# Kernel optimization log

Hardware: AMD Instinct MI355X
Metric: run time of the kernel (lower is better)

Reference implementation:

```python
import jax, jax.numpy as jnp
import numpy as np

V, E, H, B, S, T = 32000, 256, 256, 64, 512, 256


def setup_inputs() -> dict:
    key = jax.random.key(0)
    ks = jax.random.split(key, 24)
    def w(i, shape, scale=0.05):
        return jax.random.normal(ks[i], shape, jnp.float32) * scale
    return {
        "pre_seq": jax.random.randint(ks[0], (B, S), 0, V),
        "post_seq": jax.random.randint(ks[1], (B, S), 0, V),
        "trg": jax.random.randint(ks[2], (B, T), 0, V),
        "emb": w(3, (V, E)),
        "Wi_pre": w(4, (3 * H, E)), "Wh_pre": w(5, (3 * H, H)),
        "bi_pre": w(6, (3 * H,)), "bh_pre": w(7, (3 * H,)),
        "Wi_post": w(8, (3 * H, E)), "Wh_post": w(9, (3 * H, H)),
        "bi_post": w(10, (3 * H,)), "bh_post": w(11, (3 * H,)),
        "Wfc": w(12, (H, 2 * H)), "bfc": w(13, (H,)),
        "Wi_dec": w(14, (3 * H, E)), "Wh_dec": w(15, (3 * H, H)),
        "bi_dec": w(16, (3 * H,)), "bh_dec": w(17, (3 * H,)),
        "w_hid": w(18, (1, 2 * H)), "b_hid": w(19, (1,)),
        "w_out": w(20, (1, 1)), "b_out": w(21, (1,)),
    }


def gru_cell(h, x, Wi, Wh, bi, bh):
    # torch nn.GRU gating convention, gates ordered (r, z, n)
    gi = x @ Wi.T + bi              # (B, 3H)
    gh = h @ Wh.T + bh              # (B, 3H)
    ir, iz, inn = jnp.split(gi, 3, axis=-1)
    hr, hz, hn = jnp.split(gh, 3, axis=-1)
    r = jax.nn.sigmoid(ir + hr)
    z = jax.nn.sigmoid(iz + hz)
    n = jnp.tanh(inn + r * hn)
    return (1.0 - z) * n + z * h


def gru_seq(seq_emb, Wi, Wh, bi, bh):
    # seq_emb: (B, L, E) -> outputs (B, L, H), final hidden (B, H)
    h0 = jnp.zeros((seq_emb.shape[0], Wh.shape[1]), seq_emb.dtype)
    def step(h, x):
        h = gru_cell(h, x, Wi, Wh, bi, bh)
        return h, h
    hT, outs = jax.lax.scan(step, h0, jnp.swapaxes(seq_emb, 0, 1))
    return jnp.swapaxes(outs, 0, 1), hT


def reference(pre_seq, post_seq, trg, emb, Wi_pre, Wh_pre, bi_pre, bh_pre,
              Wi_post, Wh_post, bi_post, bh_post, Wfc, bfc,
              Wi_dec, Wh_dec, bi_dec, bh_dec, w_hid, b_hid, w_out, b_out):
    # Encoder: two GRUs over pre/post token embeddings (dropout off / eval mode)
    pre_out, pre_h = gru_seq(emb[pre_seq], Wi_pre, Wh_pre, bi_pre, bh_pre)
    post_out, post_h = gru_seq(emb[post_seq], Wi_post, Wh_post, bi_post, bh_post)
    enc_out = jnp.concatenate([pre_out, post_out], axis=1)          # (B, 2S, H)
    h0 = jnp.tanh(jnp.concatenate([pre_h, post_h], axis=-1) @ Wfc.T + bfc)  # (B, H)

    # fc_hid(relu(cat([enc_out, h_t]))) splits into a step-constant enc term
    # and a per-step hidden term since relu acts elementwise on the concat.
    A = jax.nn.relu(enc_out) @ w_hid[0, :H]                         # (B, 2S)

    # Teacher-forced decoder inputs: last pre token, then trg[:, :-1]
    in_toks = jnp.concatenate([pre_seq[:, -1:], trg[:, :-1]], axis=1)  # (B, T)

    def step(h, tok):
        x = emb[tok]                                                # (B, E)
        h = gru_cell(h, x, Wi_dec, Wh_dec, bi_dec, bh_dec)          # (B, H)
        s = jax.nn.relu(h) @ w_hid[0, H:]                           # (B,)
        out = (A + s[:, None] + b_hid[0]) * w_out[0, 0] + b_out[0]  # (B, 2S)
        return h, out

    _, outs = jax.lax.scan(step, h0, in_toks.T)                     # (T, B, 2S)
    outs = jnp.swapaxes(outs, 0, 1)                                 # (B, T, 2S)
    return outs[:, :, :S], outs[:, :, S:]
```

## Files before the change

kernel.cpp:

```cpp
#include <hip/hip_runtime.h>
#include <stdint.h>

typedef _Float16 f16;
typedef _Float16 half2_t __attribute__((ext_vector_type(2)));
typedef _Float16 half8_t __attribute__((ext_vector_type(8)));
typedef float    f32x4_t __attribute__((ext_vector_type(4)));
typedef uint32_t u32x32  __attribute__((ext_vector_type(32)));

constexpr int NB = 64, NS = 512, NT = 256, NE = 256, NH = 256;
constexpr int G3 = 768;

static __device__ __forceinline__ float sigm(float x){ return 1.f/(1.f+__expf(-x)); }
static __device__ __forceinline__ float tanhfast(float x){
  float e = __expf(-2.f*x);
  return (1.f-e)/(1.f+e);
}
static __device__ __forceinline__ uint32_t pack2(float a, float b){
  half2_t h; h[0]=(f16)a; h[1]=(f16)b;
  return __builtin_bit_cast(uint32_t, h);
}
static __device__ __forceinline__ float dot2f(uint32_t w, uint32_t h, float acc){
#if __has_builtin(__builtin_amdgcn_fdot2)
  return __builtin_amdgcn_fdot2(__builtin_bit_cast(half2_t,w),
                                __builtin_bit_cast(half2_t,h), acc, false);
#else
  half2_t a = __builtin_bit_cast(half2_t,w), b = __builtin_bit_cast(half2_t,h);
  return acc + (float)a[0]*(float)b[0] + (float)a[1]*(float)b[1];
#endif
}
static __device__ __forceinline__ half8_t cvt8(float4 a, float4 b){
  half8_t p;
  p[0]=(f16)a.x; p[1]=(f16)a.y; p[2]=(f16)a.z; p[3]=(f16)a.w;
  p[4]=(f16)b.x; p[5]=(f16)b.y; p[6]=(f16)b.z; p[7]=(f16)b.w;
  return p;
}

#define LOAD_W(WSRC)                                                         \
  _Pragma("unroll")                                                          \
  for (int i=0;i<32;++i){                                                    \
    wr0[i]=(WSRC)[(size_t)i*G3];          wr1[i]=(WSRC)[(size_t)(i+32)*G3];  \
    wz0[i]=(WSRC)[(size_t)i*G3+256];      wz1[i]=(WSRC)[(size_t)(i+32)*G3+256];\
    wn0[i]=(WSRC)[(size_t)i*G3+512];      wn1[i]=(WSRC)[(size_t)(i+32)*G3+512];\
  }

#define DOT_BLOCK(W_R, W_Z, W_N, HPTR)                                       \
  _Pragma("unroll")                                                          \
  for (int c=0;c<4;++c){                                                     \
    uint4 ha = *(const uint4*)((HPTR) + c*8);                                \
    uint4 hb = *(const uint4*)((HPTR) + c*8 + 4);                            \
    uint32_t hh0=ha.x,hh1=ha.y,hh2=ha.z,hh3=ha.w;                            \
    uint32_t hh4=hb.x,hh5=hb.y,hh6=hb.z,hh7=hb.w;                            \
    a0=dot2f(W_R[c*8+0],hh0,a0); a1=dot2f(W_Z[c*8+0],hh0,a1); a2=dot2f(W_N[c*8+0],hh0,a2); \
    a0=dot2f(W_R[c*8+1],hh1,a0); a1=dot2f(W_Z[c*8+1],hh1,a1); a2=dot2f(W_N[c*8+1],hh1,a2); \
    a0=dot2f(W_R[c*8+2],hh2,a0); a1=dot2f(W_Z[c*8+2],hh2,a1); a2=dot2f(W_N[c*8+2],hh2,a2); \
    a0=dot2f(W_R[c*8+3],hh3,a0); a1=dot2f(W_Z[c*8+3],hh3,a1); a2=dot2f(W_N[c*8+3],hh3,a2); \
    a0=dot2f(W_R[c*8+4],hh4,a0); a1=dot2f(W_Z[c*8+4],hh4,a1); a2=dot2f(W_N[c*8+4],hh4,a2); \
    a0=dot2f(W_R[c*8+5],hh5,a0); a1=dot2f(W_Z[c*8+5],hh5,a1); a2=dot2f(W_N[c*8+5],hh5,a2); \
    a0=dot2f(W_R[c*8+6],hh6,a0); a1=dot2f(W_Z[c*8+6],hh6,a1); a2=dot2f(W_N[c*8+6],hh6,a2); \
    a0=dot2f(W_R[c*8+7],hh7,a0); a1=dot2f(W_Z[c*8+7],hh7,a1); a2=dot2f(W_N[c*8+7],hh7,a2); \
  }

__global__ __launch_bounds__(256) void k_prep(const float* __restrict__ Wh_pre,
                                              const float* __restrict__ Wh_post,
                                              const float* __restrict__ Wh_dec,
                                              uint32_t* __restrict__ WhT_pre,
                                              uint32_t* __restrict__ WhT_post,
                                              uint32_t* __restrict__ WhT_dec,
                                              const int* __restrict__ pre_seq,
                                              const int* __restrict__ trg,
                                              int* __restrict__ in_toks){
  int bid = blockIdx.x;
  if (bid < 1152){
    const float* Wh = (bid < 384) ? Wh_pre : (bid < 768) ? Wh_post : Wh_dec;
    uint32_t* out   = (bid < 384) ? WhT_pre : (bid < 768) ? WhT_post : WhT_dec;
    int idx = (bid % 384)*256 + threadIdx.x;
    int kp = idx / G3, row = idx % G3;
    out[idx] = pack2(Wh[(size_t)row*NE + 2*kp], Wh[(size_t)row*NE + 2*kp + 1]);
  } else {
    int idx = (bid - 1152)*256 + threadIdx.x;
    int b = idx >> 8, t = idx & 255;
    in_toks[idx] = (t == 0) ? pre_seq[b*NS + NS-1] : trg[b*NT + t - 1];
  }
}

__global__ __launch_bounds__(256) void k_gemm_gi(const float* __restrict__ emb,
                                                 const int* __restrict__ toks,
                                                 const float* __restrict__ Wi,
                                                 const float* __restrict__ bi,
                                                 f16* __restrict__ out){
  __shared__ f16 As[128][72];
  __shared__ f16 Bs[128][72];
  const int tid = threadIdx.x;
  const int m0 = blockIdx.x*128, n0 = blockIdx.y*128;
  const int lane = tid & 63, wid = tid >> 6;
  const int wm = wid >> 1, wn = wid & 1;
  const int fr = lane & 15, fq = lane >> 4;

  f32x4_t acc[4][4];
  #pragma unroll
  for (int i=0;i<4;++i)
    #pragma unroll
    for (int j=0;j<4;++j){ acc[i][j][0]=0.f; acc[i][j][1]=0.f; acc[i][j][2]=0.f; acc[i][j][3]=0.f; }

  const int r = tid >> 1, hh = tid & 1;
  const int tok = toks[m0 + r];
  const float* asrc = emb + (size_t)tok*NE + hh*32;
  const float* bsrc = Wi  + (size_t)(n0 + r)*NE + hh*32;

  for (int k0 = 0; k0 < NE; k0 += 64){
    #pragma unroll
    for (int c=0;c<4;++c){
      float4 x0 = *(const float4*)(asrc + k0 + c*8);
      float4 x1 = *(const float4*)(asrc + k0 + c*8 + 4);
      *(half8_t*)&As[r][hh*32 + c*8] = cvt8(x0, x1);
      float4 y0 = *(const float4*)(bsrc + k0 + c*8);
      float4 y1 = *(const float4*)(bsrc + k0 + c*8 + 4);
      *(half8_t*)&Bs[r][hh*32 + c*8] = cvt8(y0, y1);
    }
    __syncthreads();
    #pragma unroll
    for (int kk=0; kk<2; ++kk){
      half8_t af[4], bf[4];
      #pragma unroll
      for (int m=0;m<4;++m) af[m] = *(const half8_t*)&As[wm*64 + m*16 + fr][kk*32 + fq*8];
      #pragma unroll
      for (int n=0;n<4;++n) bf[n] = *(const half8_t*)&Bs[wn*64 + n*16 + fr][kk*32 + fq*8];
      #pragma unroll
      for (int m=0;m<4;++m)
        #pragma unroll
        for (int n=0;n<4;++n)
          acc[m][n] = __builtin_amdgcn_mfma_f32_16x16x32_f16(af[m], bf[n], acc[m][n], 0,0,0);
    }
    __syncthreads();
  }
  #pragma unroll
  for (int n=0;n<4;++n){
    const int col = n0 + wn*64 + n*16 + fr;
    const float bv = bi[col];
    #pragma unroll
    for (int m=0;m<4;++m){
      const int rowb = m0 + wm*64 + m*16 + fq*4;
      #pragma unroll
      for (int j=0;j<4;++j)
        out[(size_t)(rowb + j)*G3 + col] = (f16)(acc[m][n][j] + bv);
    }
  }
}

__global__ __launch_bounds__(512, 2) void k_enc(const uint32_t* __restrict__ WhT_pre,
                                                const uint32_t* __restrict__ WhT_post,
                                                const f16* __restrict__ gi_pre,
                                                const f16* __restrict__ gi_post,
                                                const float* __restrict__ bh_pre,
                                                const float* __restrict__ bh_post,
                                                const float* __restrict__ w_hid,
                                                float* __restrict__ Abuf,
                                                float* __restrict__ preh,
                                                float* __restrict__ posth){
  __shared__ __align__(16) uint32_t h_pair[128];
  __shared__ float part[3][256];
  __shared__ float ared[4];

  const int b = blockIdx.x & 63, which = blockIdx.x >> 6;
  const int tid = threadIdx.x;
  const int n = tid & 255, half = tid >> 8;

  const uint32_t* WhT = which ? WhT_post : WhT_pre;
  const f16* gi = (which ? gi_post : gi_pre) + (size_t)b*NS*G3;
  const float* bh = which ? bh_post : bh_pre;

  u32x32 wr0, wr1, wz0, wz1, wn0, wn1;
  {
    const uint32_t* wsrc = WhT + (size_t)(half*64)*G3 + n;
    LOAD_W(wsrc);
  }
  const float bh0 = bh[n], bh1 = bh[256+n], bh2 = bh[512+n];
  const float whv = w_hid[n];
  float hreg = 0.f;
  if (tid < 128) h_pair[tid] = 0u;
  __syncthreads();

  float* Arow = Abuf + b*1024 + which*512;

  for (int t=0; t<NS; ++t){
    float g0=0.f, g1=0.f, g2=0.f;
    if (half == 0){
      const f16* gp = gi + (size_t)t*G3;
      g0 = (float)gp[n]; g1 = (float)gp[256+n]; g2 = (float)gp[512+n];
    }
    float a0=0.f, a1=0.f, a2=0.f;
    const uint32_t* hp = h_pair + half*64;
    DOT_BLOCK(wr0, wz0, wn0, hp);
    DOT_BLOCK(wr1, wz1, wn1, hp + 32);
    if (half == 1){ part[0][n]=a0; part[1][n]=a1; part[2][n]=a2; }
    __syncthreads();
    if (half == 0){
      float ghr = a0 + part[0][n] + bh0;
      float ghz = a1 + part[1][n] + bh1;
      float ghn = a2 + part[2][n] + bh2;
      float rg = sigm(g0 + ghr);
      float zg = sigm(g1 + ghz);
      float nn = tanhfast(g2 + rg*ghn);
      float hnew = (1.f - zg)*nn + zg*hreg;
      hreg = hnew;
      float hnb = __shfl_down(hnew, 1);
      if ((n & 1) == 0) h_pair[n >> 1] = pack2(hnew, hnb);
      float redv = fmaxf(hnew, 0.f) * whv;
      #pragma unroll
      for (int off=32; off; off>>=1) redv += __shfl_down(redv, off);
      if ((tid & 63) == 0) ared[tid >> 6] = redv;
    }
    __syncthreads();
    if (tid == 0) Arow[t] = ared[0]+ared[1]+ared[2]+ared[3];
  }
  if (half == 0) (which ? posth : preh)[b*NH + n] = hreg;
}

__global__ __launch_bounds__(512, 2) void k_dec(const uint32_t* __restrict__ WhT,
                                                const f16* __restrict__ gi,
                                                const float* __restrict__ bh,
                                                const float* __restrict__ w_hid,
                                                const float* __restrict__ Wfc,
                                                const float* __restrict__ bfc,
                                                const float* __restrict__ preh,
                                                const float* __restrict__ posth,
                                                float* __restrict__ sbuf){
  __shared__ __align__(16) uint32_t h_pair[128];
  __shared__ float part[3][256];
  __shared__ float ared[4];
  __shared__ float hcat[512];

  const int b = blockIdx.x;
  const int tid = threadIdx.x;
  const int n = tid & 255, half = tid >> 8;

  const float bh0 = bh[n], bh1 = bh[256+n], bh2 = bh[512+n];
  const float whv = w_hid[NH + n];
  float hreg = 0.f;

  hcat[tid] = (tid < 256) ? preh[b*NH + tid] : posth[b*NH + tid - 256];
  __syncthreads();
  {
    const float* wrow = Wfc + (size_t)n*512 + half*256;
    const float* hc = hcat + half*256;
    float acc = 0.f;
    #pragma unroll 4
    for (int j=0;j<256;j+=4){
      float4 wv = *(const float4*)(wrow + j);
      acc = fmaf(wv.x, hc[j],   acc);
      acc = fmaf(wv.y, hc[j+1], acc);
      acc = fmaf(wv.z, hc[j+2], acc);
      acc = fmaf(wv.w, hc[j+3], acc);
    }
    if (half == 1) part[0][n] = acc;
    __syncthreads();
    if (half == 0){
      float h0 = tanhfast(acc + part[0][n] + bfc[n]);
      hreg = h0;
      float hnb = __shfl_down(h0, 1);
      if ((n & 1) == 0) h_pair[n >> 1] = pack2(h0, hnb);
    }
    __syncthreads();
  }

  u32x32 wr0, wr1, wz0, wz1, wn0, wn1;
  {
    const uint32_t* wsrc = WhT + (size_t)(half*64)*G3 + n;
    LOAD_W(wsrc);
  }

  const f16* gib = gi + (size_t)b*NT*G3;
  for (int t=0; t<NT; ++t){
    float g0=0.f, g1=0.f, g2=0.f;
    if (half == 0){
      const f16* gp = gib + (size_t)t*G3;
      g0 = (float)gp[n]; g1 = (float)gp[256+n]; g2 = (float)gp[512+n];
    }
    float a0=0.f, a1=0.f, a2=0.f;
    const uint32_t* hp = h_pair + half*64;
    DOT_BLOCK(wr0, wz0, wn0, hp);
    DOT_BLOCK(wr1, wz1, wn1, hp + 32);
    if (half == 1){ part[0][n]=a0; part[1][n]=a1; part[2][n]=a2; }
    __syncthreads();
    if (half == 0){
      float ghr = a0 + part[0][n] + bh0;
      float ghz = a1 + part[1][n] + bh1;
      float ghn = a2 + part[2][n] + bh2;
      float rg = sigm(g0 + ghr);
      float zg = sigm(g1 + ghz);
      float nn = tanhfast(g2 + rg*ghn);
      float hnew = (1.f - zg)*nn + zg*hreg;
      hreg = hnew;
      float hnb = __shfl_down(hnew, 1);
      if ((n & 1) == 0) h_pair[n >> 1] = pack2(hnew, hnb);
      float redv = fmaxf(hnew, 0.f) * whv;
      #pragma unroll
      for (int off=32; off; off>>=1) redv += __shfl_down(redv, off);
      if ((tid & 63) == 0) ared[tid >> 6] = redv;
    }
    __syncthreads();
    if (tid == 0) sbuf[b*NT + t] = ared[0]+ared[1]+ared[2]+ared[3];
  }
}

__global__ __launch_bounds__(256) void k_final(const float* __restrict__ Abuf,
                                               const float* __restrict__ sbuf,
                                               const float* __restrict__ b_hid,
                                               const float* __restrict__ w_out,
                                               const float* __restrict__ b_out,
                                               float* __restrict__ out){
  const float bh = b_hid[0], wo = w_out[0], bo = b_out[0];
  const int idx = blockIdx.x*256 + threadIdx.x;
  const int j4 = idx & 127, t = (idx >> 7) & 255, b = idx >> 15;
  const float sv = sbuf[b*NT + t] + bh;
  const float4 a0 = *(const float4*)(Abuf + b*1024 + j4*4);
  const float4 a1 = *(const float4*)(Abuf + b*1024 + 512 + j4*4);
  float4 o0, o1;
  o0.x = (a0.x + sv)*wo + bo; o0.y = (a0.y + sv)*wo + bo;
  o0.z = (a0.z + sv)*wo + bo; o0.w = (a0.w + sv)*wo + bo;
  o1.x = (a1.x + sv)*wo + bo; o1.y = (a1.y + sv)*wo + bo;
  o1.z = (a1.z + sv)*wo + bo; o1.w = (a1.w + sv)*wo + bo;
  float4* o = (float4*)out;
  o[idx] = o0;
  o[(size_t)(NB*NT*NS/4) + idx] = o1;
}

extern "C" void kernel_launch(void* const* d_in, const int* in_sizes, int n_in,
                              void* d_out, int out_size, void* d_ws, size_t ws_size,
                              hipStream_t stream){
  const int*   pre_seq = (const int*)d_in[0];
  const int*   post_seq= (const int*)d_in[1];
  const int*   trg     = (const int*)d_in[2];
  const float* emb     = (const float*)d_in[3];
  const float* Wi_pre  = (const float*)d_in[4];
  const float* Wh_pre  = (const float*)d_in[5];
  const float* bi_pre  = (const float*)d_in[6];
  const float* bh_pre  = (const float*)d_in[7];
  const float* Wi_post = (const float*)d_in[8];
  const float* Wh_post = (const float*)d_in[9];
  const float* bi_post = (const float*)d_in[10];
  const float* bh_post = (const float*)d_in[11];
  const float* Wfc     = (const float*)d_in[12];
  const float* bfc     = (const float*)d_in[13];
  const float* Wi_dec  = (const float*)d_in[14];
  const float* Wh_dec  = (const float*)d_in[15];
  const float* bi_dec  = (const float*)d_in[16];
  const float* bh_dec  = (const float*)d_in[17];
  const float* w_hid   = (const float*)d_in[18];
  const float* b_hid   = (const float*)d_in[19];
  const float* w_out   = (const float*)d_in[20];
  const float* b_out   = (const float*)d_in[21];

  char* wp = (char*)d_ws;
  f16* gi_pre  = (f16*)wp; wp += (size_t)NB*NS*G3*2;
  f16* gi_post = (f16*)wp; wp += (size_t)NB*NS*G3*2;
  f16* gi_dec  = (f16*)wp; wp += (size_t)NB*NT*G3*2;
  uint32_t* WhT_pre  = (uint32_t*)wp; wp += (size_t)128*G3*4;
  uint32_t* WhT_post = (uint32_t*)wp; wp += (size_t)128*G3*4;
  uint32_t* WhT_dec  = (uint32_t*)wp; wp += (size_t)128*G3*4;
  int*   in_toks = (int*)wp;   wp += (size_t)NB*NT*4;
  float* Abuf    = (float*)wp; wp += (size_t)NB*1024*4;
  float* sbuf    = (float*)wp; wp += (size_t)NB*NT*4;
  float* preh    = (float*)wp; wp += (size_t)NB*NH*4;
  float* posth   = (float*)wp; wp += (size_t)NB*NH*4;
  (void)ws_size; (void)in_sizes; (void)n_in; (void)out_size;

  k_prep<<<1216, 256, 0, stream>>>(Wh_pre, Wh_post, Wh_dec,
                                   WhT_pre, WhT_post, WhT_dec,
                                   pre_seq, trg, in_toks);

  k_gemm_gi<<<dim3(256,6), 256, 0, stream>>>(emb, pre_seq,  Wi_pre,  bi_pre,  gi_pre);
  k_gemm_gi<<<dim3(256,6), 256, 0, stream>>>(emb, post_seq, Wi_post, bi_post, gi_post);
  k_gemm_gi<<<dim3(128,6), 256, 0, stream>>>(emb, in_toks,  Wi_dec,  bi_dec,  gi_dec);

  k_enc<<<128, 512, 0, stream>>>(WhT_pre, WhT_post, gi_pre, gi_post,
                                 bh_pre, bh_post, w_hid, Abuf, preh, posth);
  k_dec<<<64, 512, 0, stream>>>(WhT_dec, gi_dec, bh_dec, w_hid, Wfc, bfc,
                                preh, posth, sbuf);
  k_final<<<NB*NT*NS/4/256, 256, 0, stream>>>(Abuf, sbuf, b_hid, w_out, b_out,
                                              (float*)d_out);
}
```

Measured before the change: 1.280 ms.

## Split recurrent weights between pinned registers and LDS to relieve register pressure

The encoder and decoder recurrent kernels previously kept all 192 packed weight words per thread in registers, with launch bounds asking for two blocks per CU. They now pin 160 words in registers using empty asm constraints and stage the remaining 32 words of the n-gate (upper half of K) in LDS. Padding shared memory is added so only one block fits per CU. The aim is to stop register spills and scratch traffic, at the cost of extra LDS reads inside the serial time loop and lower occupancy.

```diff
diff --git a/kernel.cpp b/kernel.cpp
--- a/kernel.cpp
+++ b/kernel.cpp
@@ -5,7 +5,7 @@
 typedef _Float16 half2_t __attribute__((ext_vector_type(2)));
 typedef _Float16 half8_t __attribute__((ext_vector_type(8)));
 typedef float    f32x4_t __attribute__((ext_vector_type(4)));
-typedef uint32_t u32x32  __attribute__((ext_vector_type(32)));
+typedef uint32_t u32x4   __attribute__((ext_vector_type(4)));
 
 constexpr int NB = 64, NS = 512, NT = 256, NE = 256, NH = 256;
 constexpr int G3 = 768;
@@ -35,30 +35,55 @@
   return p;
 }
 
-#define LOAD_W(WSRC)                                                         \
+#define PINQ(g, C, RO)                                                       \
+  u32x4 q##g##_##C = { wsrc[(size_t)((C)*4+0)*G3 + (RO)],                    \
+                       wsrc[(size_t)((C)*4+1)*G3 + (RO)],                    \
+                       wsrc[(size_t)((C)*4+2)*G3 + (RO)],                    \
+                       wsrc[(size_t)((C)*4+3)*G3 + (RO)] };                  \
+  asm volatile("" : "+v"(q##g##_##C));
+
+#define PIN_ALL                                                              \
+  PINQ(0,0,0) PINQ(0,1,0) PINQ(0,2,0) PINQ(0,3,0)                            \
+  PINQ(0,4,0) PINQ(0,5,0) PINQ(0,6,0) PINQ(0,7,0)                            \
+  PINQ(0,8,0) PINQ(0,9,0) PINQ(0,10,0) PINQ(0,11,0)                          \
+  PINQ(0,12,0) PINQ(0,13,0) PINQ(0,14,0) PINQ(0,15,0)                        \
+  PINQ(1,0,256) PINQ(1,1,256) PINQ(1,2,256) PINQ(1,3,256)                    \
+  PINQ(1,4,256) PINQ(1,5,256) PINQ(1,6,256) PINQ(1,7,256)                    \
+  PINQ(1,8,256) PINQ(1,9,256) PINQ(1,10,256) PINQ(1,11,256)                  \
+  PINQ(1,12,256) PINQ(1,13,256) PINQ(1,14,256) PINQ(1,15,256)                \
+  PINQ(2,0,512) PINQ(2,1,512) PINQ(2,2,512) PINQ(2,3,512)                    \
+  PINQ(2,4,512) PINQ(2,5,512) PINQ(2,6,512) PINQ(2,7,512)
+
+#define STAGE_LW                                                             \
   _Pragma("unroll")                                                          \
-  for (int i=0;i<32;++i){                                                    \
-    wr0[i]=(WSRC)[(size_t)i*G3];          wr1[i]=(WSRC)[(size_t)(i+32)*G3];  \
-    wz0[i]=(WSRC)[(size_t)i*G3+256];      wz1[i]=(WSRC)[(size_t)(i+32)*G3+256];\
-    wn0[i]=(WSRC)[(size_t)i*G3+512];      wn1[i]=(WSRC)[(size_t)(i+32)*G3+512];\
-  }
-
-#define DOT_BLOCK(W_R, W_Z, W_N, HPTR)                                       \
-  _Pragma("unroll")                                                          \
-  for (int c=0;c<4;++c){                                                     \
-    uint4 ha = *(const uint4*)((HPTR) + c*8);                                \
-    uint4 hb = *(const uint4*)((HPTR) + c*8 + 4);                            \
-    uint32_t hh0=ha.x,hh1=ha.y,hh2=ha.z,hh3=ha.w;                            \
-    uint32_t hh4=hb.x,hh5=hb.y,hh6=hb.z,hh7=hb.w;                            \
-    a0=dot2f(W_R[c*8+0],hh0,a0); a1=dot2f(W_Z[c*8+0],hh0,a1); a2=dot2f(W_N[c*8+0],hh0,a2); \
-    a0=dot2f(W_R[c*8+1],hh1,a0); a1=dot2f(W_Z[c*8+1],hh1,a1); a2=dot2f(W_N[c*8+1],hh1,a2); \
-    a0=dot2f(W_R[c*8+2],hh2,a0); a1=dot2f(W_Z[c*8+2],hh2,a1); a2=dot2f(W_N[c*8+2],hh2,a2); \
-    a0=dot2f(W_R[c*8+3],hh3,a0); a1=dot2f(W_Z[c*8+3],hh3,a1); a2=dot2f(W_N[c*8+3],hh3,a2); \
-    a0=dot2f(W_R[c*8+4],hh4,a0); a1=dot2f(W_Z[c*8+4],hh4,a1); a2=dot2f(W_N[c*8+4],hh4,a2); \
-    a0=dot2f(W_R[c*8+5],hh5,a0); a1=dot2f(W_Z[c*8+5],hh5,a1); a2=dot2f(W_N[c*8+5],hh5,a2); \
-    a0=dot2f(W_R[c*8+6],hh6,a0); a1=dot2f(W_Z[c*8+6],hh6,a1); a2=dot2f(W_N[c*8+6],hh6,a2); \
-    a0=dot2f(W_R[c*8+7],hh7,a0); a1=dot2f(W_Z[c*8+7],hh7,a1); a2=dot2f(W_N[c*8+7],hh7,a2); \
-  }
+  for (int c=0;c<8;++c){                                                     \
+    u32x4 v = { wsrc[(size_t)((c+8)*4+0)*G3 + 512],                          \
+                wsrc[(size_t)((c+8)*4+1)*G3 + 512],                          \
+                wsrc[(size_t)((c+8)*4+2)*G3 + 512],                          \
+                wsrc[(size_t)((c+8)*4+3)*G3 + 512] };                        \
+    lw[c*512 + tid] = v;                                                     \
+  }
+
+#define CHUNKP(C) {                                                          \
+    u32x4 hq = *(const u32x4*)(hp + 4*(C));                                  \
+    a0=dot2f(q0_##C[0],hq[0],a0); a1=dot2f(q1_##C[0],hq[0],a1); a2=dot2f(q2_##C[0],hq[0],a2); \
+    a0=dot2f(q0_##C[1],hq[1],a0); a1=dot2f(q1_##C[1],hq[1],a1); a2=dot2f(q2_##C[1],hq[1],a2); \
+    a0=dot2f(q0_##C[2],hq[2],a0); a1=dot2f(q1_##C[2],hq[2],a1); a2=dot2f(q2_##C[2],hq[2],a2); \
+    a0=dot2f(q0_##C[3],hq[3],a0); a1=dot2f(q1_##C[3],hq[3],a1); a2=dot2f(q2_##C[3],hq[3],a2); }
+
+#define CHUNKM(C) {                                                          \
+    u32x4 hq = *(const u32x4*)(hp + 4*(C));                                  \
+    u32x4 wl = lwp[((C)-8)*512];                                             \
+    a0=dot2f(q0_##C[0],hq[0],a0); a1=dot2f(q1_##C[0],hq[0],a1); a2=dot2f(wl[0],hq[0],a2); \
+    a0=dot2f(q0_##C[1],hq[1],a0); a1=dot2f(q1_##C[1],hq[1],a1); a2=dot2f(wl[1],hq[1],a2); \
+    a0=dot2f(q0_##C[2],hq[2],a0); a1=dot2f(q1_##C[2],hq[2],a1); a2=dot2f(wl[2],hq[2],a2); \
+    a0=dot2f(q0_##C[3],hq[3],a0); a1=dot2f(q1_##C[3],hq[3],a1); a2=dot2f(wl[3],hq[3],a2); }
+
+#define DOT_ALL                                                              \
+  CHUNKP(0) CHUNKP(1) CHUNKP(2) CHUNKP(3)                                    \
+  CHUNKP(4) CHUNKP(5) CHUNKP(6) CHUNKP(7)                                    \
+  CHUNKM(8) CHUNKM(9) CHUNKM(10) CHUNKM(11)                                  \
+  CHUNKM(12) CHUNKM(13) CHUNKM(14) CHUNKM(15)
 
 __global__ __launch_bounds__(256) void k_prep(const float* __restrict__ Wh_pre,
                                               const float* __restrict__ Wh_post,
@@ -147,19 +172,21 @@
   }
 }
 
-__global__ __launch_bounds__(512, 2) void k_enc(const uint32_t* __restrict__ WhT_pre,
-                                                const uint32_t* __restrict__ WhT_post,
-                                                const f16* __restrict__ gi_pre,
-                                                const f16* __restrict__ gi_post,
-                                                const float* __restrict__ bh_pre,
-                                                const float* __restrict__ bh_post,
-                                                const float* __restrict__ w_hid,
-                                                float* __restrict__ Abuf,
-                                                float* __restrict__ preh,
-                                                float* __restrict__ posth){
+__global__ __launch_bounds__(512) void k_enc(const uint32_t* __restrict__ WhT_pre,
+                                             const uint32_t* __restrict__ WhT_post,
+                                             const f16* __restrict__ gi_pre,
+                                             const f16* __restrict__ gi_post,
+                                             const float* __restrict__ bh_pre,
+                                             const float* __restrict__ bh_post,
+                                             const float* __restrict__ w_hid,
+                                             float* __restrict__ Abuf,
+                                             float* __restrict__ preh,
+                                             float* __restrict__ posth){
+  __shared__ __align__(16) u32x4 lw[8*512];
   __shared__ __align__(16) uint32_t h_pair[128];
   __shared__ float part[3][256];
   __shared__ float ared[4];
+  __shared__ float pad_force[4608];
 
   const int b = blockIdx.x & 63, which = blockIdx.x >> 6;
   const int tid = threadIdx.x;
@@ -169,11 +196,11 @@
   const f16* gi = (which ? gi_post : gi_pre) + (size_t)b*NS*G3;
   const float* bh = which ? bh_post : bh_pre;
 
-  u32x32 wr0, wr1, wz0, wz1, wn0, wn1;
-  {
-    const uint32_t* wsrc = WhT + (size_t)(half*64)*G3 + n;
-    LOAD_W(wsrc);
-  }
+  const uint32_t* wsrc = WhT + (size_t)(half*64)*G3 + n;
+  PIN_ALL
+  STAGE_LW
+  if (tid == 0) pad_force[0] = 0.f;
+
   const float bh0 = bh[n], bh1 = bh[256+n], bh2 = bh[512+n];
   const float whv = w_hid[n];
   float hreg = 0.f;
@@ -181,17 +208,19 @@
   __syncthreads();
 
   float* Arow = Abuf + b*1024 + which*512;
-
+  const uint32_t* hp = h_pair + half*64;
+  const u32x4* lwp = lw + tid;
+  const f16* gp = gi + n;
+
+  #pragma unroll 1
   for (int t=0; t<NS; ++t){
     float g0=0.f, g1=0.f, g2=0.f;
     if (half == 0){
-      const f16* gp = gi + (size_t)t*G3;
-      g0 = (float)gp[n]; g1 = (float)gp[256+n]; g2 = (float)gp[512+n];
-    }
+      g0 = (float)gp[0]; g1 = (float)gp[256]; g2 = (float)gp[512];
+    }
+    gp += G3;
     float a0=0.f, a1=0.f, a2=0.f;
-    const uint32_t* hp = h_pair + half*64;
-    DOT_BLOCK(wr0, wz0, wn0, hp);
-    DOT_BLOCK(wr1, wz1, wn1, hp + 32);
+    DOT_ALL
     if (half == 1){ part[0][n]=a0; part[1][n]=a1; part[2][n]=a2; }
     __syncthreads();
     if (half == 0){
@@ -216,23 +245,30 @@
   if (half == 0) (which ? posth : preh)[b*NH + n] = hreg;
 }
 
-__global__ __launch_bounds__(512, 2) void k_dec(const uint32_t* __restrict__ WhT,
-                                                const f16* __restrict__ gi,
-                                                const float* __restrict__ bh,
-                                                const float* __restrict__ w_hid,
-                                                const float* __restrict__ Wfc,
-                                                const float* __restrict__ bfc,
-                                                const float* __restrict__ preh,
-                                                const float* __restrict__ posth,
-                                                float* __restrict__ sbuf){
+__global__ __launch_bounds__(512) void k_dec(const uint32_t* __restrict__ WhT,
+                                             const f16* __restrict__ gi,
+                                             const float* __restrict__ bh,
+                                             const float* __restrict__ w_hid,
+                                             const float* __restrict__ Wfc,
+                                             const float* __restrict__ bfc,
+                                             const float* __restrict__ preh,
+                                             const float* __restrict__ posth,
+                                             float* __restrict__ sbuf){
+  __shared__ __align__(16) u32x4 lw[8*512];
   __shared__ __align__(16) uint32_t h_pair[128];
   __shared__ float part[3][256];
   __shared__ float ared[4];
   __shared__ float hcat[512];
+  __shared__ float pad_force[4608];
 
   const int b = blockIdx.x;
   const int tid = threadIdx.x;
   const int n = tid & 255, half = tid >> 8;
+
+  const uint32_t* wsrc = WhT + (size_t)(half*64)*G3 + n;
+  PIN_ALL
+  STAGE_LW
+  if (tid == 0) pad_force[0] = 0.f;
 
   const float bh0 = bh[n], bh1 = bh[256+n], bh2 = bh[512+n];
   const float whv = w_hid[NH + n];
@@ -263,23 +299,20 @@
     __syncthreads();
   }
 
-  u32x32 wr0, wr1, wz0, wz1, wn0, wn1;
-  {
-    const uint32_t* wsrc = WhT + (size_t)(half*64)*G3 + n;
-    LOAD_W(wsrc);
-  }
-
-  const f16* gib = gi + (size_t)b*NT*G3;
+  float* srow = sbuf + b*NT;
+  const uint32_t* hp = h_pair + half*64;
+  const u32x4* lwp = lw + tid;
+  const f16* gp = gi + (size_t)b*NT*G3 + n;
+
+  #pragma unroll 1
   for (int t=0; t<NT; ++t){
     float g0=0.f, g1=0.f, g2=0.f;
     if (half == 0){
-      const f16* gp = gib + (size_t)t*G3;
-      g0 = (float)gp[n]; g1 = (float)gp[256+n]; g2 = (float)gp[512+n];
-    }
+      g0 = (float)gp[0]; g1 = (float)gp[256]; g2 = (float)gp[512];
+    }
+    gp += G3;
     float a0=0.f, a1=0.f, a2=0.f;
-    const uint32_t* hp = h_pair + half*64;
-    DOT_BLOCK(wr0, wz0, wn0, hp);
-    DOT_BLOCK(wr1, wz1, wn1, hp + 32);
+    DOT_ALL
     if (half == 1){ part[0][n]=a0; part[1][n]=a1; part[2][n]=a2; }
     __syncthreads();
     if (half == 0){
@@ -299,7 +332,7 @@
       if ((tid & 63) == 0) ared[tid >> 6] = redv;
     }
     __syncthreads();
-    if (tid == 0) sbuf[b*NT + t] = ared[0]+ared[1]+ared[2]+ared[3];
+    if (tid == 0) srow[t] = ared[0]+ared[1]+ared[2]+ared[3];
   }
 }
 
```

After: 1.314 ms. 2.7% more time.
